# Optimization experiments

Measured on AMD Instinct MI355X. Metric: run time of the kernel, lower is better.

Reference implementation:

```python
import jax, jax.numpy as jnp
import numpy as np

VOCAB, EMB, HID, NTAG, SEQ = 50000, 256, 512, 20, 8192
H = HID // 2  # per-direction hidden size


def _lstm_dir(x, Wih, Whh, bih, bhh, reverse):
    # x: [S, E]; PyTorch gate order i, f, g, o
    h0 = jnp.zeros((H,), x.dtype)
    c0 = jnp.zeros((H,), x.dtype)
    b = bih + bhh
    xg = x @ Wih.T + b  # [S, 4H] precompute input projection

    def step(carry, xt):
        h, c = carry
        gates = xt + h @ Whh.T
        i, f, g, o = jnp.split(gates, 4)
        i = jax.nn.sigmoid(i)
        f = jax.nn.sigmoid(f)
        g = jnp.tanh(g)
        o = jax.nn.sigmoid(o)
        c = f * c + i * g
        h = o * jnp.tanh(c)
        return (h, c), h

    _, hs = jax.lax.scan(step, (h0, c0), xg, reverse=reverse)
    return hs  # [S, H]


def _viterbi(emissions, start_trans, end_trans, trans):
    # emissions [S, T]; torchcrf-style Viterbi decode
    score0 = start_trans + emissions[0]

    def fwd(score, em):
        tot = score[:, None] + trans          # [T_from, T_to]
        bp = jnp.argmax(tot, axis=0)          # best previous tag per next tag
        score = jnp.max(tot, axis=0) + em
        return score, bp

    final, bps = jax.lax.scan(fwd, score0, emissions[1:])
    final = final + end_trans
    last = jnp.argmax(final).astype(jnp.int32)

    def back(tag, bp):
        prev = bp[tag].astype(jnp.int32)
        return prev, prev

    _, prevs = jax.lax.scan(back, last, bps, reverse=True)
    return jnp.concatenate([prevs, last[None]])  # [S]


def setup_inputs() -> dict:
    key = jax.random.key(0)
    ks = jax.random.split(key, 16)
    s = 0.1
    inp = {
        "sentence": jax.random.randint(ks[0], (SEQ,), 0, VOCAB, dtype=jnp.int64)
                    if jax.config.read("jax_enable_x64") else
                    jax.random.randint(ks[0], (SEQ,), 0, VOCAB, dtype=jnp.int32),
        "embed": jax.random.normal(ks[1], (VOCAB, EMB), jnp.float32),
        "Wih_f": jax.random.normal(ks[2], (4 * H, EMB), jnp.float32) * s,
        "Whh_f": jax.random.normal(ks[3], (4 * H, H), jnp.float32) * s,
        "bih_f": jax.random.normal(ks[4], (4 * H,), jnp.float32) * s,
        "bhh_f": jax.random.normal(ks[5], (4 * H,), jnp.float32) * s,
        "Wih_b": jax.random.normal(ks[6], (4 * H, EMB), jnp.float32) * s,
        "Whh_b": jax.random.normal(ks[7], (4 * H, H), jnp.float32) * s,
        "bih_b": jax.random.normal(ks[8], (4 * H,), jnp.float32) * s,
        "bhh_b": jax.random.normal(ks[9], (4 * H,), jnp.float32) * s,
        "Wout": jax.random.normal(ks[10], (NTAG, HID), jnp.float32) * s,
        "bout": jax.random.normal(ks[11], (NTAG,), jnp.float32) * s,
        "start_trans": jax.random.normal(ks[12], (NTAG,), jnp.float32) * s,
        "end_trans": jax.random.normal(ks[13], (NTAG,), jnp.float32) * s,
        "trans": jax.random.normal(ks[14], (NTAG, NTAG), jnp.float32) * s,
    }
    return inp


def reference(sentence, embed, Wih_f, Whh_f, bih_f, bhh_f,
              Wih_b, Whh_b, bih_b, bhh_b, Wout, bout,
              start_trans, end_trans, trans):
    x = embed[sentence]                                  # [S, E]
    h_f = _lstm_dir(x, Wih_f, Whh_f, bih_f, bhh_f, reverse=False)
    h_b = _lstm_dir(x, Wih_b, Whh_b, bih_b, bhh_b, reverse=True)
    lstm_out = jnp.concatenate([h_f, h_b], axis=-1)      # [S, HID]; dropout is eval-mode identity
    emissions = lstm_out @ Wout.T + bout                 # [S, T]
    path = _viterbi(emissions, start_trans, end_trans, trans)
    return path
```

## Files before the change

kernel.cpp:

```cpp
#include <hip/hip_runtime.h>
#include <hip/hip_bf16.h>


#define S    8192
#define E    256
#define Hh   256
#define G    1024
#define NT   20
#define NB   4
#define NCHUNK 128
#define CLEN   64

__global__ __launch_bounds__(1024) void pbuf_clear(unsigned long long* __restrict__ pbuf)
{
    int i = blockIdx.x * 1024 + threadIdx.x;
    if (i < 2 * 2 * NB * 1024) pbuf[i] = 0ull;
}

__global__ __launch_bounds__(1024, 4) void xg_project(
    const int* __restrict__ sent, const float* __restrict__ embed,
    const float* __restrict__ Wih_f, const float* __restrict__ bih_f, const float* __restrict__ bhh_f,
    const float* __restrict__ Wih_b, const float* __restrict__ bih_b, const float* __restrict__ bhh_b,
    float* __restrict__ xg)
{
    const int tb  = blockIdx.x;
    const int rb  = blockIdx.y;
    const int dir = blockIdx.z;
    const int tid = threadIdx.x;
    const int q   = tid >> 8;
    const int idx = tid & 255;
    const int r   = rb * 256 + idx;
    const float* Wih = dir ? Wih_b : Wih_f;

    __shared__ __align__(16) float4 xs4[32 * 64];
    __shared__ float psum[1024];

    const int t0 = tb * 32;
    #pragma unroll
    for (int i = 0; i < 2; ++i) {
        int qq  = i * 1024 + tid;
        int row = qq >> 6;
        int c4  = qq & 63;
        int widx = sent[t0 + row];
        xs4[qq] = *(const float4*)(embed + (size_t)widx * E + (size_t)c4 * 4);
    }

    float w[64];
    #pragma unroll
    for (int k = 0; k < 64; k += 4) {
        float4 v = *(const float4*)(Wih + (size_t)r * E + q * 64 + k);
        w[k] = v.x; w[k+1] = v.y; w[k+2] = v.z; w[k+3] = v.w;
    }
    float bias = 0.f;
    if (tid < 256) bias = dir ? (bih_b[r] + bhh_b[r]) : (bih_f[r] + bhh_f[r]);
    __syncthreads();

    const float* xs = (const float*)xs4 + q * 64;
    float* outb = xg + ((size_t)dir * S + t0) * G + r;
    for (int tt = 0; tt < 32; ++tt) {
        float a0 = 0.f, a1 = 0.f, a2 = 0.f, a3 = 0.f;
        #pragma unroll
        for (int k = 0; k < 64; k += 4) {
            float4 h4 = *(const float4*)(xs + tt * E + k);
            a0 = fmaf(w[k],   h4.x, a0);
            a1 = fmaf(w[k+1], h4.y, a1);
            a2 = fmaf(w[k+2], h4.z, a2);
            a3 = fmaf(w[k+3], h4.w, a3);
        }
        psum[tid] = (a0 + a1) + (a2 + a3);
        __syncthreads();
        if (tid < 256)
            outb[(size_t)tt * G] = bias +
                ((psum[idx] + psum[idx + 256]) + (psum[idx + 512] + psum[idx + 768]));
        __syncthreads();
    }
}

__global__ __launch_bounds__(1024, 4) void lstm_scan_k(
    const float* __restrict__ xg,
    const float* __restrict__ Whh_f,
    const float* __restrict__ Whh_b,
    float* __restrict__ out,
    unsigned long long* __restrict__ pbuf)
{
    const int b    = blockIdx.x;
    const int dir  = blockIdx.y;
    const int tid  = threadIdx.x;
    const float* W   = dir ? Whh_b : Whh_f;
    const float* xgd = xg + (size_t)dir * S * G;

    float w[64];
    #pragma unroll
    for (int k = 0; k < 64; k += 4) {
        float4 v = *(const float4*)(W + (size_t)tid * Hh + b * 64 + k);
        w[k] = v.x; w[k+1] = v.y; w[k+2] = v.z; w[k+3] = v.w;
    }

    __shared__ __align__(16) float h_lds[64];
    __shared__ float gl[256];
    const bool cons = (((tid >> 6) & 3) == b);
    const int  u    = tid & 63;
    const int  gate = tid >> 8;
    if (tid < 64) h_lds[tid] = 0.f;
    float c = 0.f;

    const int t0 = dir ? (S - 1) : 0;
    const int dt = dir ? -1 : 1;
    float xg_c = 0.f, xg_n1 = 0.f;
    if (cons) {
        xg_c  = xgd[(size_t)t0 * G + tid];
        xg_n1 = xgd[(size_t)(t0 + dt) * G + tid];
    }
    const int p0 = (b + 1) & 3, p1 = (b + 2) & 3, p2 = (b + 3) & 3;
    __syncthreads();

    for (int s = 0; s < S; ++s) {
        const int t = t0 + dt * s;
        float xg_n2 = 0.f;
        if (cons && s + 2 < S) xg_n2 = xgd[(size_t)(t + 2 * dt) * G + tid];

        float a0 = 0.f, a1 = 0.f, a2 = 0.f, a3 = 0.f;
        #pragma unroll
        for (int k = 0; k < 64; k += 4) {
            float4 h4 = *(const float4*)(h_lds + k);
            a0 = fmaf(w[k],   h4.x, a0);
            a1 = fmaf(w[k+1], h4.y, a1);
            a2 = fmaf(w[k+2], h4.z, a2);
            a3 = fmaf(w[k+3], h4.w, a3);
        }
        const float part = (a0 + a1) + (a2 + a3);

        const unsigned st = (unsigned)(s + 1);
        const size_t base = (size_t)((dir * 2) + (s & 1)) * (NB * 1024);
        unsigned long long pw =
            ((unsigned long long)st << 32) | (unsigned long long)__float_as_uint(part);
        __hip_atomic_store(&pbuf[base + (size_t)b * 1024 + tid], pw,
                           __ATOMIC_RELAXED, __HIP_MEMORY_SCOPE_AGENT);

        if (cons) {
            const unsigned long long* q0 = &pbuf[base + (size_t)p0 * 1024 + tid];
            const unsigned long long* q1 = &pbuf[base + (size_t)p1 * 1024 + tid];
            const unsigned long long* q2 = &pbuf[base + (size_t)p2 * 1024 + tid];
            unsigned long long u0, u1, u2;
            do {
                u0 = __hip_atomic_load(q0, __ATOMIC_RELAXED, __HIP_MEMORY_SCOPE_AGENT);
                u1 = __hip_atomic_load(q1, __ATOMIC_RELAXED, __HIP_MEMORY_SCOPE_AGENT);
                u2 = __hip_atomic_load(q2, __ATOMIC_RELAXED, __HIP_MEMORY_SCOPE_AGENT);
            } while ((unsigned)(u0 >> 32) != st || (unsigned)(u1 >> 32) != st ||
                     (unsigned)(u2 >> 32) != st);
            float acc = xg_c + part;
            acc += __uint_as_float((unsigned)u0);
            acc += __uint_as_float((unsigned)u1);
            acc += __uint_as_float((unsigned)u2);
            float a = (gate == 2) ? tanhf(acc) : 1.f / (1.f + expf(-acc));
            gl[gate * 64 + u] = a;
        }
        __syncthreads();

        if (tid < 64) {
            float iv = gl[tid];
            float fv = gl[64 + tid];
            float gv = gl[128 + tid];
            float ov = gl[192 + tid];
            c = fv * c + iv * gv;
            float h = ov * tanhf(c);
            h_lds[tid] = h;
            out[(size_t)t * 512 + dir * Hh + b * 64 + tid] = h;
        }
        __syncthreads();
        xg_c = xg_n1; xg_n1 = xg_n2;
    }
}

__global__ __launch_bounds__(256) void emissions_kernel(
    const float* __restrict__ lo,
    const float* __restrict__ Wout,
    const float* __restrict__ bout,
    float* __restrict__ em)
{
    int gid = blockIdx.x * blockDim.x + threadIdx.x;
    if (gid >= S * NT) return;
    int t = gid / NT;
    int j = gid - t * NT;
    const float* x = lo + (size_t)t * 512;
    const float* w = Wout + (size_t)j * 512;
    float a0 = 0.f, a1 = 0.f, a2 = 0.f, a3 = 0.f;
    #pragma unroll 8
    for (int k = 0; k < 512; k += 4) {
        float4 xv = *(const float4*)(x + k);
        float4 wv = *(const float4*)(w + k);
        a0 = fmaf(xv.x, wv.x, a0);
        a1 = fmaf(xv.y, wv.y, a1);
        a2 = fmaf(xv.z, wv.z, a2);
        a3 = fmaf(xv.w, wv.w, a3);
    }
    em[gid] = bout[j] + ((a0 + a1) + (a2 + a3));
}

__global__ __launch_bounds__(64) void viterbi_fwd(
    const float* __restrict__ em,
    const float* __restrict__ start_trans,
    const float* __restrict__ end_trans,
    const float* __restrict__ trans,
    unsigned char* __restrict__ bp,
    int* __restrict__ last_out)
{
    const int lane = threadIdx.x;
    const int g    = lane / 20;
    const int j    = lane - g * 20;
    const int i0   = g * 7;

    float tc[7];
    #pragma unroll
    for (int u = 0; u < 7; ++u) {
        int i = i0 + u;
        tc[u] = (g < 3 && i < 20) ? trans[i * NT + j] : -3.0e38f;
    }

    const int jj = (g < 3) ? j : 0;
    float snew  = start_trans[jj] + em[jj];
    if (g == 0) bp[j] = (unsigned char)j;
    float e_cur = em[NT + jj];

    for (int t = 1; t < S; ++t) {
        float s_sub[7];
        #pragma unroll
        for (int u = 0; u < 7; ++u)
            s_sub[u] = __shfl(snew, i0 + u);
        float e_nxt = (t + 1 < S) ? em[(size_t)(t + 1) * NT + jj] : 0.f;

        float bv = s_sub[0] + tc[0];
        int   bi = i0;
        #pragma unroll
        for (int u = 1; u < 7; ++u) {
            float v = s_sub[u] + tc[u];
            if (v > bv) { bv = v; bi = i0 + u; }
        }
        float v0 = __shfl(bv, jj), v1 = __shfl(bv, jj + 20), v2 = __shfl(bv, jj + 40);
        int   c0 = __shfl(bi, jj), c1 = __shfl(bi, jj + 20), c2 = __shfl(bi, jj + 40);
        float best = v0; int bidx = c0;
        if (v1 > best) { best = v1; bidx = c1; }
        if (v2 > best) { best = v2; bidx = c2; }
        snew = best + e_cur;
        if (g == 0) bp[(size_t)t * NT + j] = (unsigned char)bidx;
        e_cur = e_nxt;
    }

    float bv = __shfl(snew, 0) + end_trans[0];
    int   bi = 0;
    #pragma unroll 1
    for (int i = 1; i < 20; ++i) {
        float v = __shfl(snew, i) + end_trans[i];
        if (v > bv) { bv = v; bi = i; }
    }
    if (lane == 0) *last_out = bi;
}

__global__ __launch_bounds__(64) void bt_maps(
    const unsigned char* __restrict__ bp, unsigned char* __restrict__ maps)
{
    __shared__ unsigned char lbp[CLEN * NT];
    const int c = blockIdx.x, tid = threadIdx.x;
    const unsigned* src = (const unsigned*)(bp + (size_t)c * CLEN * NT);
    unsigned* dst = (unsigned*)lbp;
    for (int q = tid; q < CLEN * NT / 4; q += 64) dst[q] = src[q];
    __syncthreads();
    if (tid < NT) {
        int x = tid;
        for (int t = CLEN - 1; t >= 0; --t) x = lbp[t * NT + x];
        maps[c * NT + tid] = (unsigned char)x;
    }
}

__global__ __launch_bounds__(64) void bt_boundary(
    const unsigned char* __restrict__ maps, const int* __restrict__ last_out,
    int* __restrict__ btags)
{
    __shared__ unsigned char m[NCHUNK * NT];
    const int tid = threadIdx.x;
    for (int q = tid; q < NCHUNK * NT; q += 64) m[q] = maps[q];
    __syncthreads();
    if (tid == 0) {
        int x = *last_out;
        btags[NCHUNK - 1] = x;
        for (int c = NCHUNK - 1; c >= 1; --c) {
            x = m[c * NT + x];
            btags[c - 1] = x;
        }
    }
}

__global__ __launch_bounds__(64) void bt_emit(
    const unsigned char* __restrict__ bp, const int* __restrict__ btags,
    int* __restrict__ path)
{
    __shared__ unsigned char lbp[CLEN * NT];
    const int c = blockIdx.x, tid = threadIdx.x;
    const unsigned* src = (const unsigned*)(bp + (size_t)c * CLEN * NT);
    unsigned* dst = (unsigned*)lbp;
    for (int q = tid; q < CLEN * NT / 4; q += 64) dst[q] = src[q];
    __syncthreads();
    if (tid == 0) {
        int x = btags[c];
        path[c * CLEN + CLEN - 1] = x;
        for (int t = CLEN - 1; t >= 1; --t) {
            x = lbp[t * NT + x];
            path[c * CLEN + t - 1] = x;
        }
    }
}

extern "C" void kernel_launch(void* const* d_in, const int* in_sizes, int n_in,
                              void* d_out, int out_size, void* d_ws, size_t ws_size,
                              hipStream_t stream) {
    const int*   sent   = (const int*)  d_in[0];
    const float* embed  = (const float*)d_in[1];
    const float* Wih_f  = (const float*)d_in[2];
    const float* Whh_f  = (const float*)d_in[3];
    const float* bih_f  = (const float*)d_in[4];
    const float* bhh_f  = (const float*)d_in[5];
    const float* Wih_b  = (const float*)d_in[6];
    const float* Whh_b  = (const float*)d_in[7];
    const float* bih_b  = (const float*)d_in[8];
    const float* bhh_b  = (const float*)d_in[9];
    const float* Wout   = (const float*)d_in[10];
    const float* bout   = (const float*)d_in[11];
    const float* start_trans = (const float*)d_in[12];
    const float* end_trans   = (const float*)d_in[13];
    const float* trans       = (const float*)d_in[14];
    int* path = (int*)d_out;

    char* ws = (char*)d_ws;
    size_t off = 0;
    float* xg = (float*)(ws + off); off += (size_t)2 * S * G * 4;
    float* lo = (float*)(ws + off); off += (size_t)S * 512 * 4;
    float* em = (float*)(ws + off); off += (size_t)S * NT * 4;
    unsigned char* bp   = (unsigned char*)(ws + off); off += (size_t)S * NT;
    unsigned char* maps = (unsigned char*)(ws + off); off += 4096;
    int* btags = (int*)(ws + off); off += 1024;
    int* lastp = (int*)(ws + off); off += 256;
    off = (off + 255) & ~(size_t)255;
    unsigned long long* pbuf = (unsigned long long*)(ws + off); off += 2 * 2 * NB * 1024 * 8;

    pbuf_clear<<<dim3(16), 1024, 0, stream>>>(pbuf);
    xg_project<<<dim3(S / 32, 4, 2), 1024, 0, stream>>>(
        sent, embed, Wih_f, bih_f, bhh_f, Wih_b, bih_b, bhh_b, xg);
    lstm_scan_k<<<dim3(NB, 2), 1024, 0, stream>>>(xg, Whh_f, Whh_b, lo, pbuf);
    emissions_kernel<<<dim3((S * NT + 255) / 256), 256, 0, stream>>>(lo, Wout, bout, em);
    viterbi_fwd<<<dim3(1), 64, 0, stream>>>(em, start_trans, end_trans, trans, bp, lastp);
    bt_maps<<<dim3(NCHUNK), 64, 0, stream>>>(bp, maps);
    bt_boundary<<<dim3(1), 64, 0, stream>>>(maps, lastp, btags);
    bt_emit<<<dim3(NCHUNK), 64, 0, stream>>>(bp, btags, path);
}
```

Before: 18.10 ms.

## Partition LSTM scan by hidden units and exchange h via slots

Restructures the recurrent LSTM scan so each of 8 blocks owns 32 hidden units of both directions, instead of each of 4 blocks per direction owning a K-slice of the matvec. Blocks now exchange only their new h values (32 per direction) through flag-tagged global slots, replacing the exchange of 1024 partial gate sums per block per step. Gate nonlinearities and the cell update are done in-block with wave shuffles. The aim is to cut the per-step cross-block traffic and polling latency that dominate the serial scan. The cost is extra in-block LDS reductions and two barriers per step.

```diff
diff --git a/kernel.cpp b/kernel.cpp
--- a/kernel.cpp
+++ b/kernel.cpp
@@ -7,14 +7,13 @@
 #define Hh   256
 #define G    1024
 #define NT   20
-#define NB   4
+#define NBI  8
 #define NCHUNK 128
 #define CLEN   64
 
-__global__ __launch_bounds__(1024) void pbuf_clear(unsigned long long* __restrict__ pbuf)
-{
-    int i = blockIdx.x * 1024 + threadIdx.x;
-    if (i < 2 * 2 * NB * 1024) pbuf[i] = 0ull;
+__global__ __launch_bounds__(1024) void init_slots(unsigned long long* __restrict__ sl)
+{
+    sl[threadIdx.x] = 0ull;
 }
 
 __global__ __launch_bounds__(1024, 4) void xg_project(
@@ -76,96 +75,120 @@
     }
 }
 
-__global__ __launch_bounds__(1024, 4) void lstm_scan_k(
+__global__ __launch_bounds__(1024, 4) void lstm_scan_il(
     const float* __restrict__ xg,
     const float* __restrict__ Whh_f,
     const float* __restrict__ Whh_b,
     float* __restrict__ out,
-    unsigned long long* __restrict__ pbuf)
+    unsigned long long* __restrict__ slots)
 {
     const int b    = blockIdx.x;
-    const int dir  = blockIdx.y;
     const int tid  = threadIdx.x;
-    const float* W   = dir ? Whh_b : Whh_f;
-    const float* xgd = xg + (size_t)dir * S * G;
-
-    float w[64];
+    const int kq   = tid >> 7;
+    const int ridx = tid & 127;
+    const int gate = ridx & 3;
+    const int hloc = ridx >> 2;
+    const int row  = gate * Hh + b * 32 + hloc;
+
+    float w0[32], w1[32];
     #pragma unroll
-    for (int k = 0; k < 64; k += 4) {
-        float4 v = *(const float4*)(W + (size_t)tid * Hh + b * 64 + k);
-        w[k] = v.x; w[k+1] = v.y; w[k+2] = v.z; w[k+3] = v.w;
-    }
-
-    __shared__ __align__(16) float h_lds[64];
-    __shared__ float gl[256];
-    const bool cons = (((tid >> 6) & 3) == b);
-    const int  u    = tid & 63;
-    const int  gate = tid >> 8;
-    if (tid < 64) h_lds[tid] = 0.f;
-    float c = 0.f;
-
-    const int t0 = dir ? (S - 1) : 0;
-    const int dt = dir ? -1 : 1;
+    for (int k = 0; k < 32; k += 4) {
+        float4 v = *(const float4*)(Whh_f + (size_t)row * Hh + kq * 32 + k);
+        w0[k] = v.x; w0[k+1] = v.y; w0[k+2] = v.z; w0[k+3] = v.w;
+        float4 u = *(const float4*)(Whh_b + (size_t)row * Hh + kq * 32 + k);
+        w1[k] = u.x; w1[k+1] = u.y; w1[k+2] = u.z; w1[k+3] = u.w;
+    }
+
+    __shared__ __align__(16) float h0[Hh], h1[Hh];
+    __shared__ float ps0[1024], ps1[1024];
+    if (tid < Hh) { h0[tid] = 0.f; h1[tid] = 0.f; }
+    float cc = 0.f;
+
+    const bool isRed = (tid < 256);
+    const int  rd    = (tid >> 7) & 1;
+    const int  rr    = tid & 127;
+    const int  rg    = rr & 3;
+    const int  rh    = rr >> 2;
+    const int  rrow  = rg * Hh + b * 32 + rh;
+    const int  rdt   = rd ? -1 : 1;
+    const int  rt0   = rd ? (S - 1) : 0;
+    const float* xgp = xg + (size_t)rd * S * G + rrow;
+
+    const bool isPol = (tid >= 256 && tid < 704);
+    const int  pl    = tid - 256;
+    const int  pd    = (pl >= 224) ? 1 : 0;
+    const int  pq    = pd ? (pl - 224) : pl;
+    const int  peer  = pq >> 5;
+    const int  word  = pq & 31;
+    const int  pb    = peer + (peer >= b);
+
     float xg_c = 0.f, xg_n1 = 0.f;
-    if (cons) {
-        xg_c  = xgd[(size_t)t0 * G + tid];
-        xg_n1 = xgd[(size_t)(t0 + dt) * G + tid];
-    }
-    const int p0 = (b + 1) & 3, p1 = (b + 2) & 3, p2 = (b + 3) & 3;
+    if (isRed) {
+        xg_c  = xgp[(size_t)rt0 * G];
+        xg_n1 = xgp[(size_t)(rt0 + rdt) * G];
+    }
     __syncthreads();
 
     for (int s = 0; s < S; ++s) {
-        const int t = t0 + dt * s;
         float xg_n2 = 0.f;
-        if (cons && s + 2 < S) xg_n2 = xgd[(size_t)(t + 2 * dt) * G + tid];
-
+        if (isRed && s + 2 < S)
+            xg_n2 = xgp[(size_t)(rt0 + rdt * (s + 2)) * G];
+
+        const float* hp0 = (const float*)h0 + kq * 32;
+        const float* hp1 = (const float*)h1 + kq * 32;
         float a0 = 0.f, a1 = 0.f, a2 = 0.f, a3 = 0.f;
+        float b0 = 0.f, b1 = 0.f, b2 = 0.f, b3 = 0.f;
         #pragma unroll
-        for (int k = 0; k < 64; k += 4) {
-            float4 h4 = *(const float4*)(h_lds + k);
-            a0 = fmaf(w[k],   h4.x, a0);
-            a1 = fmaf(w[k+1], h4.y, a1);
-            a2 = fmaf(w[k+2], h4.z, a2);
-            a3 = fmaf(w[k+3], h4.w, a3);
-        }
-        const float part = (a0 + a1) + (a2 + a3);
-
-        const unsigned st = (unsigned)(s + 1);
-        const size_t base = (size_t)((dir * 2) + (s & 1)) * (NB * 1024);
-        unsigned long long pw =
-            ((unsigned long long)st << 32) | (unsigned long long)__float_as_uint(part);
-        __hip_atomic_store(&pbuf[base + (size_t)b * 1024 + tid], pw,
-                           __ATOMIC_RELAXED, __HIP_MEMORY_SCOPE_AGENT);
-
-        if (cons) {
-            const unsigned long long* q0 = &pbuf[base + (size_t)p0 * 1024 + tid];
-            const unsigned long long* q1 = &pbuf[base + (size_t)p1 * 1024 + tid];
-            const unsigned long long* q2 = &pbuf[base + (size_t)p2 * 1024 + tid];
-            unsigned long long u0, u1, u2;
+        for (int k = 0; k < 32; k += 4) {
+            float4 x4 = *(const float4*)(hp0 + k);
+            a0 = fmaf(w0[k],   x4.x, a0);
+            a1 = fmaf(w0[k+1], x4.y, a1);
+            a2 = fmaf(w0[k+2], x4.z, a2);
+            a3 = fmaf(w0[k+3], x4.w, a3);
+            float4 y4 = *(const float4*)(hp1 + k);
+            b0 = fmaf(w1[k],   y4.x, b0);
+            b1 = fmaf(w1[k+1], y4.y, b1);
+            b2 = fmaf(w1[k+2], y4.z, b2);
+            b3 = fmaf(w1[k+3], y4.w, b3);
+        }
+        ps0[tid] = (a0 + a1) + (a2 + a3);
+        ps1[tid] = (b0 + b1) + (b2 + b3);
+        __syncthreads();
+
+        const unsigned st  = (unsigned)(s + 1);
+        const int      par = s & 1;
+
+        if (isRed) {
+            const float* ps = rd ? ps1 : ps0;
+            float s0 = ps[rr]       + ps[rr + 128];
+            float s1 = ps[rr + 256] + ps[rr + 384];
+            float s2 = ps[rr + 512] + ps[rr + 640];
+            float s3 = ps[rr + 768] + ps[rr + 896];
+            float acc = xg_c + ((s0 + s1) + (s2 + s3));
+            float a = (rg == 2) ? tanhf(acc) : 1.f / (1.f + expf(-acc));
+            float fv = __shfl_down(a, 1);
+            float gv = __shfl_down(a, 2);
+            float ov = __shfl_down(a, 3);
+            if (rg == 0) {
+                cc = fv * cc + a * gv;
+                float h = ov * tanhf(cc);
+                const int t = rt0 + rdt * s;
+                unsigned long long pw = ((unsigned long long)st << 32) |
+                                        (unsigned long long)__float_as_uint(h);
+                __hip_atomic_store(&slots[((rd * 2 + par) * NBI + b) * 32 + rh],
+                                   pw, __ATOMIC_RELAXED, __HIP_MEMORY_SCOPE_AGENT);
+                out[(size_t)t * 512 + rd * Hh + b * 32 + rh] = h;
+                (rd ? h1 : h0)[b * 32 + rh] = h;
+            }
+        } else if (isPol && s + 1 < S) {
+            unsigned long long* sp =
+                &slots[((pd * 2 + par) * NBI + pb) * 32 + word];
+            unsigned long long v;
             do {
-                u0 = __hip_atomic_load(q0, __ATOMIC_RELAXED, __HIP_MEMORY_SCOPE_AGENT);
-                u1 = __hip_atomic_load(q1, __ATOMIC_RELAXED, __HIP_MEMORY_SCOPE_AGENT);
-                u2 = __hip_atomic_load(q2, __ATOMIC_RELAXED, __HIP_MEMORY_SCOPE_AGENT);
-            } while ((unsigned)(u0 >> 32) != st || (unsigned)(u1 >> 32) != st ||
-                     (unsigned)(u2 >> 32) != st);
-            float acc = xg_c + part;
-            acc += __uint_as_float((unsigned)u0);
-            acc += __uint_as_float((unsigned)u1);
-            acc += __uint_as_float((unsigned)u2);
-            float a = (gate == 2) ? tanhf(acc) : 1.f / (1.f + expf(-acc));
-            gl[gate * 64 + u] = a;
-        }
-        __syncthreads();
-
-        if (tid < 64) {
-            float iv = gl[tid];
-            float fv = gl[64 + tid];
-            float gv = gl[128 + tid];
-            float ov = gl[192 + tid];
-            c = fv * c + iv * gv;
-            float h = ov * tanhf(c);
-            h_lds[tid] = h;
-            out[(size_t)t * 512 + dir * Hh + b * 64 + tid] = h;
+                v = __hip_atomic_load(sp, __ATOMIC_RELAXED,
+                                      __HIP_MEMORY_SCOPE_AGENT);
+            } while ((unsigned)(v >> 32) != st);
+            (pd ? h1 : h0)[pb * 32 + word] = __uint_as_float((unsigned)v);
         }
         __syncthreads();
         xg_c = xg_n1; xg_n1 = xg_n2;
@@ -340,12 +363,12 @@
     int* btags = (int*)(ws + off); off += 1024;
     int* lastp = (int*)(ws + off); off += 256;
     off = (off + 255) & ~(size_t)255;
-    unsigned long long* pbuf = (unsigned long long*)(ws + off); off += 2 * 2 * NB * 1024 * 8;
-
-    pbuf_clear<<<dim3(16), 1024, 0, stream>>>(pbuf);
+    unsigned long long* slots = (unsigned long long*)(ws + off); off += 1024 * 8;
+
+    init_slots<<<dim3(1), 1024, 0, stream>>>(slots);
     xg_project<<<dim3(S / 32, 4, 2), 1024, 0, stream>>>(
         sent, embed, Wih_f, bih_f, bhh_f, Wih_b, bih_b, bhh_b, xg);
-    lstm_scan_k<<<dim3(NB, 2), 1024, 0, stream>>>(xg, Whh_f, Whh_b, lo, pbuf);
+    lstm_scan_il<<<dim3(NBI), 1024, 0, stream>>>(xg, Whh_f, Whh_b, lo, slots);
     emissions_kernel<<<dim3((S * NT + 255) / 256), 256, 0, stream>>>(lo, Wout, bout, em);
     viterbi_fwd<<<dim3(1), 64, 0, stream>>>(em, start_trans, end_trans, trans, bp, lastp);
     bt_maps<<<dim3(NCHUNK), 64, 0, stream>>>(bp, maps);
```

Result: no change. 17.90 ms (-1.1%).
